# Performance work log

Hardware: AMD Instinct MI355X
Metric: run time of the kernel (lower is better)

The kernel has to match this reference:

```python
import jax, jax.numpy as jnp
import numpy as np


def _gru_dir(x, Wih, Whh, bih, bhh):
    # x: (B,T,I) -> (B,T,H); torch GRU equations, h0 = 0
    H = Whh.shape[1]
    pre = x @ Wih.T + bih  # (B,T,3H), input projection hoisted out of scan
    def step(h, p):
        gh = h @ Whh.T + bhh
        pr, pz, pn = jnp.split(p, 3, axis=-1)
        gr, gz, gn = jnp.split(gh, 3, axis=-1)
        r = jax.nn.sigmoid(pr + gr)
        z = jax.nn.sigmoid(pz + gz)
        n = jnp.tanh(pn + r * gn)
        h = (1.0 - z) * n + z * h
        return h, h
    h0 = jnp.zeros((x.shape[0], H), x.dtype)
    _, ys = jax.lax.scan(step, h0, jnp.swapaxes(pre, 0, 1))
    return jnp.swapaxes(ys, 0, 1)


def _gru_bidir(x, Wih, Whh, bih, bhh):
    f = _gru_dir(x, Wih[0], Whh[0], bih[0], bhh[0])
    b = _gru_dir(x[:, ::-1], Wih[1], Whh[1], bih[1], bhh[1])[:, ::-1]
    return jnp.concatenate([f, b], axis=-1)


def _forward(inputs, embed, l_Wih, l_Whh, l_bih, l_bhh, r_Wih, r_Whh, r_bih, r_bhh,
             a_Wih, a_Whh, a_bih, a_bhh, Wc1, Wc2, vc, Wb, Wd, vd, Wm, vm, Ws, vs,
             Wp, vp, Wpred):
    x = embed[inputs]  # (B,T,E)
    hl = _gru_bidir(x, l_Wih, l_Whh, l_bih, l_bhh)  # (B,T,2H)
    hr = _gru_bidir(x, r_Wih, r_Whh, r_bih, r_bhh)  # (B,T,2H)
    # co-attention: score[b,i,j] = vc . tanh(Wc1 hl_j + Wc2 hr_i)
    s = jnp.tanh((hl @ Wc1.T)[:, None, :, :] + (hr @ Wc2.T)[:, :, None, :])  # (B,T,T,H)
    ptc = jax.nn.softmax((s @ vc.T)[..., 0], axis=-1) @ hl
    # bilinear: hr (Wb hl)^T
    sjt = jnp.einsum('bid,bjd->bij', hr, hl @ Wb.T)
    ptb = jax.nn.softmax(sjt, axis=-1) @ hl
    # multiplicative: vd . tanh(Wd (hl_j * hr_i))
    p = hl[:, None, :, :] * hr[:, :, None, :]  # (B,T,T,2H)
    ptd = jax.nn.softmax((jnp.tanh(p @ Wd.T) @ vd.T)[..., 0], axis=-1) @ hl
    # subtractive: vm . tanh(Wm (hl_j - hr_i))
    d = hl[:, None, :, :] - hr[:, :, None, :]  # (B,T,T,2H)
    ptm = jax.nn.softmax((jnp.tanh(d @ Wm.T) @ vm.T)[..., 0], axis=-1) @ hl
    # self-attention on hr: vs . tanh(Ws (hr_j * hr_i))
    ss = hr[:, None, :, :] * hr[:, :, None, :]  # (B,T,T,2H)
    pts = jax.nn.softmax((jnp.tanh(ss @ Ws.T) @ vs.T)[..., 0], axis=-1) @ hr
    agg = jnp.concatenate([hr, pts, ptc, ptd, ptb, ptm], axis=-1)  # (B,T,12H)
    ar = _gru_bidir(agg, a_Wih, a_Whh, a_bih, a_bhh)  # (B,T,2H)
    # pooling of hl
    sj = jax.nn.softmax(jnp.swapaxes(jnp.tanh(hl @ Wp.T) @ vp.T, 1, 2), axis=-1)  # (B,1,T)
    rl = sj @ hl  # (B,1,2H)
    # final attention over aggregation
    sj2 = jax.nn.softmax(jnp.swapaxes((ar @ Wc1.T + rl @ Wc2.T) @ vc.T, 1, 2), axis=-1)  # (B,1,T)
    rr = (sj2 @ ar)[:, 0, :]  # (B,2H)
    return jax.nn.sigmoid(rr @ Wpred.T)  # (B,labels)


def setup_inputs() -> dict:
    B, T, V, E, H, L = 4, 256, 30000, 300, 128, 2
    key = jax.random.key(0)
    ks = jax.random.split(key, 40)
    inp = {}
    inp['inputs'] = jax.random.randint(ks[0], (B, T), 0, V)
    inp['embed'] = jax.random.uniform(ks[1], (V, E), jnp.float32, -0.1, 0.1)
    ki = 2
    for name, isz in [('l', E), ('r', E), ('a', 12 * H)]:
        inp[name + '_Wih'] = jax.random.normal(ks[ki], (2, 3 * H, isz), jnp.float32) * 0.05; ki += 1
        inp[name + '_Whh'] = jax.random.normal(ks[ki], (2, 3 * H, H), jnp.float32) * 0.05; ki += 1
        inp[name + '_bih'] = jnp.zeros((2, 3 * H), jnp.float32)
        inp[name + '_bhh'] = jnp.zeros((2, 3 * H), jnp.float32)
    for n, o, i in [('Wc1', H, 2 * H), ('Wc2', H, 2 * H), ('vc', 1, H), ('Wb', 2 * H, 2 * H),
                    ('Wd', H, 2 * H), ('vd', 1, H), ('Wm', H, 2 * H), ('vm', 1, H),
                    ('Ws', H, 2 * H), ('vs', 1, H), ('Wp', H, 2 * H), ('vp', 1, H),
                    ('Wpred', L, 2 * H)]:
        inp[n] = jax.random.normal(ks[ki], (o, i), jnp.float32) * 0.05; ki += 1
    return inp


def reference(inputs, embed, l_Wih, l_Whh, l_bih, l_bhh, r_Wih, r_Whh, r_bih, r_bhh,
              a_Wih, a_Whh, a_bih, a_bhh, Wc1, Wc2, vc, Wb, Wd, vd, Wm, vm, Ws, vs,
              Wp, vp, Wpred):
    return _forward(inputs, embed, l_Wih, l_Whh, l_bih, l_bhh, r_Wih, r_Whh, r_bih,
                    r_bhh, a_Wih, a_Whh, a_bih, a_bhh, Wc1, Wc2, vc, Wb, Wd, vd, Wm,
                    vm, Ws, vs, Wp, vp, Wpred)
```

## Files before the change

### kernel.cpp

```cpp
#include <hip/hip_runtime.h>


#define DEV static __device__ __forceinline__
#define BAR_LGKM() __asm__ volatile("s_waitcnt lgkmcnt(0)\ns_barrier" ::: "memory")

typedef __attribute__((ext_vector_type(4))) float f32x4;
typedef __attribute__((ext_vector_type(8))) short s16x8;
typedef __attribute__((ext_vector_type(4))) unsigned int u32x4;

constexpr int T = 256, E = 300, EP = 320, H = 128, H2 = 256, H3 = 384, H12 = 1536;
constexpr int M = 1024;
constexpr int STY = 262144;

DEV float b2f(unsigned short h) { return __uint_as_float(((unsigned)h) << 16); }
DEV unsigned short f2b(float f) {
  unsigned u = __float_as_uint(f);
  u += 0x7fff + ((u >> 16) & 1);
  return (unsigned short)(u >> 16);
}
DEV unsigned cvt_pk_bf16(float lo, float hi) {
  unsigned r;
  __asm__("v_cvt_pk_bf16_f32 %0, %1, %2" : "=v"(r) : "v"(lo), "v"(hi));
  return r;
}
DEV float rcp_f(float x) {
  float r;
  __asm__("v_rcp_f32 %0, %1" : "=v"(r) : "v"(x));
  return r;
}
DEV float sigm(float x) { return rcp_f(1.f + __expf(-x)); }
DEV float tanh_f(float x) {
  float e = __expf(2.f * x);
  return __builtin_fmaf(-2.f, rcp_f(e + 1.f), 1.f);
}

DEV s16x8 ldfrag(const unsigned short* p) {
  u32x4 v = *(const u32x4*)p;
  return __builtin_bit_cast(s16x8, v);
}
DEV f32x4 mfma16(s16x8 a, s16x8 b, f32x4 c) {
  return __builtin_amdgcn_mfma_f32_16x16x32_bf16(a, b, c, 0, 0, 0);
}


struct StageArgs {
  const float* cs[9]; unsigned short* cd[9]; int cn[9];
  const int* idx; const float* emb; unsigned short* xhi; unsigned short* xlo;
  const float* lW; const float* rW; unsigned short* wpad;
};

__global__ void k_stage(StageArgs sa) {
  int seg = blockIdx.y;
  int i = blockIdx.x * 256 + threadIdx.x;
  if (seg < 9) {
    if (i < sa.cn[seg]) sa.cd[seg][i] = f2b(sa.cs[seg][i]);
    return;
  }
  if (seg == 9) {
    if (i >= M * EP) return;
    int m = i / EP, e = i - m * EP;
    int r = sa.idx[m];
    float v = (e < E) ? sa.emb[(size_t)r * E + e] : 0.f;
    unsigned short hi = f2b(v);
    sa.xhi[i] = hi;
    sa.xlo[i] = f2b(v - b2f(hi));
    return;
  }
  if (i >= 4 * H3 * EP) return;
  int e = i % EP, n = (i / EP) % H3, uu = i / (EP * H3);
  const float* src = (uu < 2 ? sa.lW : sa.rW) + (size_t)((uu & 1) * H3 + n) * E;
  sa.wpad[i] = (e < E) ? f2b(src[e]) : (unsigned short)0;
}


struct GemmDesc {
  const unsigned short* Ahi; const unsigned short* Alo; const unsigned short* W;
  const float* bias; float* Cf; int N; int K; int tr;
};
struct GemmBatch { GemmDesc d[8]; };

__global__ __launch_bounds__(256) void k_gemm(GemmBatch gb) {
  GemmDesc g = gb.d[blockIdx.z];
  int nb = blockIdx.y * 64;
  if (nb >= g.N) return;
  int mb = blockIdx.x * 64;
  int lane = threadIdx.x & 63, w = threadIdx.x >> 6, quad = lane >> 4, l16 = lane & 15;
  int K = g.K;
  const unsigned short* Ahp = g.Ahi + (size_t)(mb + w * 16 + l16) * K + quad * 8;
  const unsigned short* Alp = g.Alo + (size_t)(mb + w * 16 + l16) * K + quad * 8;
  const unsigned short* Wp = g.W + (size_t)(nb + l16) * K + quad * 8;
  f32x4 acc[4];
  #pragma unroll
  for (int nt = 0; nt < 4; ++nt) acc[nt] = f32x4{0.f, 0.f, 0.f, 0.f};
  for (int k = 0; k < K; k += 32) {
    s16x8 ah = ldfrag(Ahp + k);
    s16x8 al = ldfrag(Alp + k);
    #pragma unroll
    for (int nt = 0; nt < 4; ++nt) {
      s16x8 b = ldfrag(Wp + (size_t)nt * 16 * K + k);
      acc[nt] = mfma16(ah, b, acc[nt]);
      acc[nt] = mfma16(al, b, acc[nt]);
    }
  }
  int mr0 = mb + w * 16 + quad * 4;
  #pragma unroll
  for (int nt = 0; nt < 4; ++nt) {
    int col = nb + nt * 16 + l16;
    float bv = g.bias ? g.bias[col] : 0.f;
    #pragma unroll
    for (int r = 0; r < 4; ++r) {
      if (g.tr)
        g.Cf[(size_t)col * M + (mr0 + r)] = acc[nt][r] + bv;
      else
        g.Cf[(size_t)(mr0 + r) * g.N + col] = acc[nt][r] + bv;
    }
  }
}


struct RecArgs {
  const unsigned short* whh[4];
  const float* pre[4];
  float* outf[4];
  unsigned short* outhi[4];
  unsigned short* outlo[4];
  unsigned short* agghi[4];
  unsigned short* agglo[4];
  const float* bhh[4];
  int colOff[4];
  int dir[4];
};

__global__ __launch_bounds__(512) void k_gru(RecArgs ra) {
  int u = blockIdx.x;
  __shared__ __align__(16) unsigned short hs[2][16 * 136];
  int tid = threadIdx.x, lane = tid & 63, w8 = tid >> 6;
  int quad = lane >> 4, l16 = lane & 15;
  for (int i = tid; i < 2 * 16 * 136; i += 512) ((unsigned short*)hs)[i] = 0;
  const unsigned short* whh = ra.whh[u];
  s16x8 bq[3][4];
  #pragma unroll
  for (int g = 0; g < 3; ++g) {
    int row = g * 128 + w8 * 16 + l16;
    #pragma unroll
    for (int kc = 0; kc < 4; ++kc)
      bq[g][kc] = ldfrag(whh + (size_t)row * H + kc * 32 + quad * 8);
  }
  const float* bhh = ra.bhh[u];
  const float* pre = ra.pre[u];
  float* outf = ra.outf[u];
  unsigned short* outhi = ra.outhi[u];
  unsigned short* outlo = ra.outlo[u];
  unsigned short* agghi = ra.agghi[u];
  unsigned short* agglo = ra.agglo[u];
  int colOff = ra.colOff[u], dir = ra.dir[u];
  int b = ((quad & 1) << 1) | (quad >> 1);
  int d = w8 * 16 + l16;
  float bh_r = bhh[d], bh_z = bhh[d + 128], bh_n = bhh[d + 256];
  float hf = 0.f;
  float ob[8];
  unsigned short obh[8], obl[8];
  int t0 = dir ? (T - 1) : 0;
  const float* pq = pre + (size_t)(b * T + t0) * H3 + d;
  float n_pr = pq[0], n_pz = pq[128], n_pn = pq[256];
  long pst = dir ? -(long)H3 : (long)H3;
  __syncthreads();
  for (int sb = 0; sb < T; sb += 8) {
    #pragma unroll
    for (int ss = 0; ss < 8; ++ss) {
      float pr = n_pr, pz = n_pz, pn = n_pn;
      pq += pst;
      n_pr = pq[0]; n_pz = pq[128]; n_pn = pq[256];
      const unsigned short* hcur = hs[ss & 1];
      unsigned short* hnxt = hs[(ss & 1) ^ 1];
      s16x8 ah[4];
      #pragma unroll
      for (int kc = 0; kc < 4; ++kc)
        ah[kc] = ldfrag(hcur + l16 * 136 + kc * 32 + quad * 8);
      f32x4 accA[3], accB[3];
      #pragma unroll
      for (int g = 0; g < 3; ++g) {
        accA[g] = f32x4{0.f, 0.f, 0.f, 0.f};
        accB[g] = f32x4{0.f, 0.f, 0.f, 0.f};
      }
      #pragma unroll
      for (int g = 0; g < 3; ++g) accA[g] = mfma16(ah[0], bq[g][0], accA[g]);
      #pragma unroll
      for (int g = 0; g < 3; ++g) accB[g] = mfma16(ah[2], bq[g][2], accB[g]);
      #pragma unroll
      for (int g = 0; g < 3; ++g) accA[g] = mfma16(ah[1], bq[g][1], accA[g]);
      #pragma unroll
      for (int g = 0; g < 3; ++g) accB[g] = mfma16(ah[3], bq[g][3], accB[g]);
      float ghv[3];
      #pragma unroll
      for (int g = 0; g < 3; ++g) {
        float x0 = (accA[g][0] + accB[g][0]) + (accA[g][1] + accB[g][1]);
        float x1 = (accA[g][2] + accB[g][2]) + (accA[g][3] + accB[g][3]);
        float y1 = __shfl_xor(x1, 32);
        ghv[g] = (quad >= 2) ? y1 : x0;
      }
      float rg = sigm(pr + ghv[0] + bh_r);
      float zg = sigm(pz + ghv[1] + bh_z);
      float ng = tanh_f(pn + rg * (ghv[2] + bh_n));
      hf = (1.f - zg) * ng + zg * hf;
      unsigned short hi = f2b(hf);
      unsigned short lo = f2b(hf - b2f(hi));
      hnxt[(2 * b) * 136 + d] = hi;
      hnxt[(2 * b + 1) * 136 + d] = lo;
      ob[ss] = hf; obh[ss] = hi; obl[ss] = lo;
      BAR_LGKM();
    }
    #pragma unroll
    for (int qq = 0; qq < 8; ++qq) {
      int sq = sb + qq;
      int tq = dir ? (T - 1 - sq) : sq;
      size_t o = (size_t)(b * T + tq) * H2 + colOff + d;
      outf[o] = ob[qq]; outhi[o] = obh[qq]; outlo[o] = obl[qq];
      if (agghi) {
        size_t a = (size_t)(b * T + tq) * H12 + colOff + d;
        agghi[a] = obh[qq]; agglo[a] = obl[qq];
      }
    }
  }
}


struct ScMMArgs {
  const unsigned short* Xhi[2];
  const float* Rf; const float* Wt[2]; const float* vt[2];
  float* So[2]; float* So2[2];
};

__global__ __launch_bounds__(256, 2) void k_scmm(ScMMArgs a) {
  __shared__ __align__(16) unsigned short w_lds[64 * 256];
  int which = blockIdx.y;
  int bi = blockIdx.x, b = bi >> 8;
  int tid = threadIdx.x;
  int type = which >> 1, khb = which & 1;
  const unsigned short* Xhi = a.Xhi[type];
  const float* W = a.Wt[type] + (size_t)khb * 64 * 256;
  const float* v = a.vt[type] + khb * 64;
  float* Sout = khb ? a.So2[type] : a.So[type];
  int lane = tid & 63, w = tid >> 6, quad = lane >> 4, l16 = lane & 15;
  int d4 = tid & 63, rhi = tid >> 6;
  float4 h4 = ((const float4*)(a.Rf + (size_t)bi * 256))[d4];
  #pragma unroll
  for (int it = 0; it < 16; ++it) {
    int kl = it * 4 + rhi;
    float4 w4 = ((const float4*)(W + (size_t)kl * 256))[d4];
    unsigned lo32 = cvt_pk_bf16(w4.x * h4.x, w4.y * h4.y);
    unsigned hi32 = cvt_pk_bf16(w4.z * h4.z, w4.w * h4.w);
    unsigned long long pk = (unsigned long long)lo32 | ((unsigned long long)hi32 << 32);
    int gphys = ((d4 >> 1) + kl) & 31;
    *(unsigned long long*)(w_lds + (size_t)kl * 256 + gphys * 8 + (d4 & 1) * 4) = pk;
  }
  BAR_LGKM();
  f32x4 acc[4][4];
  #pragma unroll
  for (int jj = 0; jj < 4; ++jj)
    #pragma unroll
    for (int c = 0; c < 4; ++c) acc[jj][c] = f32x4{0.f, 0.f, 0.f, 0.f};
  const unsigned short* Xp0 =
      Xhi + (size_t)(b * 256 + w * 4 * 16 + l16) * 256 + quad * 8;
  #pragma unroll 2
  for (int kc = 0; kc < 8; ++kc) {
    s16x8 af[4];
    #pragma unroll
    for (int c = 0; c < 4; ++c) {
      int krow = c * 16 + l16;
      int gp = (kc * 4 + quad + krow) & 31;
      af[c] = ldfrag(w_lds + (size_t)krow * 256 + gp * 8);
    }
    s16x8 bf[4];
    #pragma unroll
    for (int jj = 0; jj < 4; ++jj)
      bf[jj] = ldfrag(Xp0 + (size_t)jj * 16 * 256 + kc * 32);
    #pragma unroll
    for (int jj = 0; jj < 4; ++jj)
      #pragma unroll
      for (int c = 0; c < 4; ++c)
        acc[jj][c] = mfma16(af[c], bf[jj], acc[jj][c]);
  }
  float vv[4][4];
  #pragma unroll
  for (int c = 0; c < 4; ++c)
    #pragma unroll
    for (int r = 0; r < 4; ++r) vv[c][r] = v[c * 16 + quad * 4 + r];
  #pragma unroll
  for (int jj = 0; jj < 4; ++jj) {
    float s = 0.f;
    #pragma unroll
    for (int c = 0; c < 4; ++c)
      #pragma unroll
      for (int r = 0; r < 4; ++r) s += tanh_f(acc[jj][c][r]) * vv[c][r];
    s += __shfl_xor(s, 16);
    s += __shfl_xor(s, 32);
    int jt = w * 4 + jj;
    if (lane < 16) Sout[(size_t)bi * 256 + jt * 16 + l16] = s;
  }
}


struct ScCmbArgs {
  const float *Hc, *Rc, *Hm, *Rm, *HB, *hrf, *vcf, *vmf; float* S;
};

__global__ __launch_bounds__(256, 2) void k_sccmb(ScCmbArgs a) {
  int bi = blockIdx.x;
  int tid = threadIdx.x;
  __shared__ float rc_l[8 * 128];
  __shared__ float rm_l[8 * 128];
  __shared__ float hr_l[8 * 256];
  __shared__ float vc_l[128], vm_l[128];
  int b = bi >> 5, i0 = (bi & 31) << 3;
  int gi0 = b * 256 + i0;
  {
    const float4* rc4 = (const float4*)(a.Rc + (size_t)gi0 * 128);
    const float4* rm4 = (const float4*)(a.Rm + (size_t)gi0 * 128);
    ((float4*)rc_l)[tid] = rc4[tid];
    ((float4*)rm_l)[tid] = rm4[tid];
    const float4* hr4 = (const float4*)(a.hrf + (size_t)gi0 * 256);
    ((float4*)hr_l)[tid] = hr4[tid];
    ((float4*)hr_l)[256 + tid] = hr4[256 + tid];
    if (tid < 128) { vc_l[tid] = a.vcf[tid]; vm_l[tid] = a.vmf[tid]; }
  }
  __syncthreads();
  int j = tid;
  size_t cb = (size_t)(b * 256 + j);
  float scq[8], smq[8], sbq[8];
  #pragma unroll
  for (int q = 0; q < 8; ++q) { scq[q] = 0.f; smq[q] = 0.f; sbq[q] = 0.f; }
  for (int k = 0; k < 128; ++k) {
    float hc = a.Hc[(size_t)k * M + cb];
    float hm = a.Hm[(size_t)k * M + cb];
    float vck = vc_l[k], vmk = vm_l[k];
    #pragma unroll
    for (int q = 0; q < 8; ++q) {
      scq[q] += vck * tanh_f(hc + rc_l[q * 128 + k]);
      smq[q] += vmk * tanh_f(hm - rm_l[q * 128 + k]);
    }
  }
  for (int k = 0; k < 256; ++k) {
    float hb = a.HB[(size_t)k * M + cb];
    #pragma unroll
    for (int q = 0; q < 8; ++q) sbq[q] += hb * hr_l[q * 256 + k];
  }
  #pragma unroll
  for (int q = 0; q < 8; ++q) {
    size_t o = (size_t)(gi0 + q) * 256 + j;
    a.S[(size_t)STY * 1 + o] = scq[q];
    a.S[(size_t)STY * 3 + o] = sbq[q];
    a.S[(size_t)STY * 4 + o] = smq[q];
  }
}


__global__ __launch_bounds__(256) void k_wsum(const float* __restrict__ S,
    const float* __restrict__ S2,
    const float* __restrict__ hl_f, const float* __restrict__ hr_f,
    unsigned short* __restrict__ ahi, unsigned short* __restrict__ alo) {
  int it = blockIdx.x, type = blockIdx.y, b = blockIdx.z;
  __shared__ float p_l[8][256];
  __shared__ float red[4];
  int tid = threadIdx.x;
  for (int ii = 0; ii < 8; ++ii) {
    size_t idx = ((size_t)(b * 256 + it * 8 + ii)) * 256 + tid;
    float x = S[(size_t)type * STY + idx];
    if (type == 0) x += S2[idx];
    else if (type == 2) x += S2[(size_t)STY + idx];
    float m = x;
    for (int dl = 32; dl; dl >>= 1) m = fmaxf(m, __shfl_xor(m, dl));
    if ((tid & 63) == 0) red[tid >> 6] = m;
    __syncthreads();
    m = fmaxf(fmaxf(red[0], red[1]), fmaxf(red[2], red[3]));
    __syncthreads();
    float e = __expf(x - m);
    float sum = e;
    for (int dl = 32; dl; dl >>= 1) sum += __shfl_xor(sum, dl);
    if ((tid & 63) == 0) red[tid >> 6] = sum;
    __syncthreads();
    sum = red[0] + red[1] + red[2] + red[3];
    p_l[ii][tid] = e * rcp_f(sum);
    __syncthreads();
  }
  const float* src = (type == 0 ? hr_f : hl_f) + (size_t)b * 256 * 256;
  float acc[8] = {0.f, 0.f, 0.f, 0.f, 0.f, 0.f, 0.f, 0.f};
  for (int j = 0; j < 256; ++j) {
    float hv = src[(size_t)j * 256 + tid];
    #pragma unroll
    for (int ii = 0; ii < 8; ++ii) acc[ii] += p_l[ii][j] * hv;
  }
  int off = 256 * (1 + type);
  #pragma unroll
  for (int ii = 0; ii < 8; ++ii) {
    float vv = acc[ii];
    unsigned short hi = f2b(vv);
    size_t o = (size_t)(b * 256 + it * 8 + ii) * H12 + off + tid;
    ahi[o] = hi;
    alo[o] = f2b(vv - b2f(hi));
  }
}


__global__ __launch_bounds__(256) void k_tail(const float* __restrict__ Hp,
    const float* __restrict__ hl_f, const float* __restrict__ vpf,
    const float* __restrict__ Wc2f, const float* __restrict__ Arc,
    const float* __restrict__ ar_f, const float* __restrict__ vcf,
    const float* __restrict__ Wpredf, float* __restrict__ out) {
  int b = blockIdx.x, tid = threadIdx.x;
  __shared__ float vl[128], wl[256], rvec[256], rlcl[128], red[4];
  if (tid < 128) vl[tid] = vpf[tid];
  __syncthreads();
  const float* hp = Hp + (size_t)(b * 256 + tid) * 128;
  float s = 0.f;
  for (int k = 0; k < 128; ++k) s += vl[k] * tanh_f(hp[k]);
  float m = s;
  for (int dl = 32; dl; dl >>= 1) m = fmaxf(m, __shfl_xor(m, dl));
  if ((tid & 63) == 0) red[tid >> 6] = m;
  __syncthreads();
  m = fmaxf(fmaxf(red[0], red[1]), fmaxf(red[2], red[3]));
  __syncthreads();
  float e = __expf(s - m);
  float sum = e;
  for (int dl = 32; dl; dl >>= 1) sum += __shfl_xor(sum, dl);
  if ((tid & 63) == 0) red[tid >> 6] = sum;
  __syncthreads();
  sum = red[0] + red[1] + red[2] + red[3];
  wl[tid] = e * rcp_f(sum);
  __syncthreads();
  float acc = 0.f;
  for (int t = 0; t < 256; ++t) acc += wl[t] * hl_f[(size_t)(b * 256 + t) * 256 + tid];
  rvec[tid] = acc;
  __syncthreads();
  if (tid < 128) {
    float a2 = 0.f;
    const float* wr = Wc2f + (size_t)tid * 256;
    for (int dk = 0; dk < 256; ++dk) a2 += rvec[dk] * wr[dk];
    rlcl[tid] = a2;
    vl[tid] = vcf[tid];
  }
  __syncthreads();
  const float* ap = Arc + (size_t)(b * 256 + tid) * 128;
  float s2 = 0.f;
  for (int k = 0; k < 128; ++k) s2 += vl[k] * (ap[k] + rlcl[k]);
  m = s2;
  for (int dl = 32; dl; dl >>= 1) m = fmaxf(m, __shfl_xor(m, dl));
  if ((tid & 63) == 0) red[tid >> 6] = m;
  __syncthreads();
  m = fmaxf(fmaxf(red[0], red[1]), fmaxf(red[2], red[3]));
  __syncthreads();
  float e2 = __expf(s2 - m);
  float sum2 = e2;
  for (int dl = 32; dl; dl >>= 1) sum2 += __shfl_xor(sum2, dl);
  if ((tid & 63) == 0) red[tid >> 6] = sum2;
  __syncthreads();
  sum2 = red[0] + red[1] + red[2] + red[3];
  wl[tid] = e2 * rcp_f(sum2);
  __syncthreads();
  float acc2 = 0.f;
  for (int t = 0; t < 256; ++t) acc2 += wl[t] * ar_f[(size_t)(b * 256 + t) * 256 + tid];
  rvec[tid] = acc2;
  __syncthreads();
  if (tid < 2) {
    float o = 0.f;
    const float* wp = Wpredf + (size_t)tid * 256;
    for (int dk = 0; dk < 256; ++dk) o += rvec[dk] * wp[dk];
    out[b * 2 + tid] = sigm(o);
  }
}


extern "C" void kernel_launch(void* const* d_in, const int* in_sizes, int n_in,
                              void* d_out, int out_size, void* d_ws, size_t ws_size,
                              hipStream_t stream) {
  (void)in_sizes; (void)n_in; (void)out_size; (void)ws_size;
  const int* inputs = (const int*)d_in[0];
  const float* embed = (const float*)d_in[1];
  const float* lWih = (const float*)d_in[2];
  const float* lWhh = (const float*)d_in[3];
  const float* lbih = (const float*)d_in[4];
  const float* lbhh = (const float*)d_in[5];
  const float* rWih = (const float*)d_in[6];
  const float* rWhh = (const float*)d_in[7];
  const float* rbih = (const float*)d_in[8];
  const float* rbhh = (const float*)d_in[9];
  const float* aWih = (const float*)d_in[10];
  const float* aWhh = (const float*)d_in[11];
  const float* abih = (const float*)d_in[12];
  const float* abhh = (const float*)d_in[13];
  const float* Wc1 = (const float*)d_in[14];
  const float* Wc2 = (const float*)d_in[15];
  const float* vc  = (const float*)d_in[16];
  const float* Wb  = (const float*)d_in[17];
  const float* Wd  = (const float*)d_in[18];
  const float* vd  = (const float*)d_in[19];
  const float* Wm  = (const float*)d_in[20];
  const float* vmv = (const float*)d_in[21];
  const float* Wsw = (const float*)d_in[22];
  const float* vsv = (const float*)d_in[23];
  const float* Wp  = (const float*)d_in[24];
  const float* vp  = (const float*)d_in[25];
  const float* Wpred = (const float*)d_in[26];

  char* ws = (char*)d_ws;
  size_t off = 0;
  auto alloc = [&](size_t bytes) -> void* {
    void* p = ws + off;
    off += (bytes + 255) & ~(size_t)255;
    return p;
  };
  unsigned short* xhi = (unsigned short*)alloc((size_t)M * EP * 2);
  unsigned short* xlo = (unsigned short*)alloc((size_t)M * EP * 2);
  unsigned short* wpad = (unsigned short*)alloc((size_t)4 * H3 * EP * 2);
  unsigned short* Whh_b = (unsigned short*)alloc((size_t)6 * H3 * H * 2);
  unsigned short* aWih_b = (unsigned short*)alloc((size_t)2 * H3 * H12 * 2);
  unsigned short* Wc1_b = (unsigned short*)alloc((size_t)H * H2 * 2);
  unsigned short* Wc2_b = (unsigned short*)alloc((size_t)H * H2 * 2);
  unsigned short* Wm_b  = (unsigned short*)alloc((size_t)H * H2 * 2);
  unsigned short* Wp_b  = (unsigned short*)alloc((size_t)H * H2 * 2);
  unsigned short* Wb_b  = (unsigned short*)alloc((size_t)H2 * H2 * 2);
  char* region1 = (char*)alloc((size_t)4 * M * H3 * 4);
  float* pre_lr = (float*)region1;
  float* S      = (float*)region1;
  float* pre_a  = (float*)region1;
  float* S2 = (float*)alloc((size_t)2 * STY * 4);
  float* hl_f = (float*)alloc((size_t)M * H2 * 4);
  float* hr_f = (float*)alloc((size_t)M * H2 * 4);
  unsigned short* hl_hi = (unsigned short*)alloc((size_t)M * H2 * 2);
  unsigned short* hl_lo = (unsigned short*)alloc((size_t)M * H2 * 2);
  unsigned short* hr_hi = (unsigned short*)alloc((size_t)M * H2 * 2);
  unsigned short* hr_lo = (unsigned short*)alloc((size_t)M * H2 * 2);
  float* Hc = (float*)alloc((size_t)M * H * 4);
  float* Rc = (float*)alloc((size_t)M * H * 4);
  float* Hm = (float*)alloc((size_t)M * H * 4);
  float* Rm = (float*)alloc((size_t)M * H * 4);
  float* Hp = (float*)alloc((size_t)M * H * 4);
  float* HB = (float*)alloc((size_t)M * H2 * 4);
  unsigned short* agg_hi = (unsigned short*)alloc((size_t)M * H12 * 2);
  unsigned short* agg_lo = (unsigned short*)alloc((size_t)M * H12 * 2);
  float* ar_f = (float*)alloc((size_t)M * H2 * 4);
  unsigned short* ar_hi = (unsigned short*)alloc((size_t)M * H2 * 2);
  unsigned short* ar_lo = (unsigned short*)alloc((size_t)M * H2 * 2);
  float* Arc = (float*)alloc((size_t)M * H * 4);

  StageArgs sa{};
  sa.cs[0] = lWhh;  sa.cd[0] = Whh_b;                 sa.cn[0] = 2 * H3 * H;
  sa.cs[1] = rWhh;  sa.cd[1] = Whh_b + 2 * H3 * H;    sa.cn[1] = 2 * H3 * H;
  sa.cs[2] = aWhh;  sa.cd[2] = Whh_b + 4 * H3 * H;    sa.cn[2] = 2 * H3 * H;
  sa.cs[3] = aWih;  sa.cd[3] = aWih_b;                sa.cn[3] = 2 * H3 * H12;
  sa.cs[4] = Wc1;   sa.cd[4] = Wc1_b;                 sa.cn[4] = H * H2;
  sa.cs[5] = Wc2;   sa.cd[5] = Wc2_b;                 sa.cn[5] = H * H2;
  sa.cs[6] = Wm;    sa.cd[6] = Wm_b;                  sa.cn[6] = H * H2;
  sa.cs[7] = Wp;    sa.cd[7] = Wp_b;                  sa.cn[7] = H * H2;
  sa.cs[8] = Wb;    sa.cd[8] = Wb_b;                  sa.cn[8] = H2 * H2;
  sa.idx = inputs; sa.emb = embed; sa.xhi = xhi; sa.xlo = xlo;
  sa.lW = lWih; sa.rW = rWih; sa.wpad = wpad;
  k_stage<<<dim3((2 * H3 * H12 + 255) / 256, 11), dim3(256), 0, stream>>>(sa);

  GemmBatch ga{};
  const float* biases[4] = { lbih, lbih + H3, rbih, rbih + H3 };
  for (int u = 0; u < 4; ++u)
    ga.d[u] = GemmDesc{ xhi, xlo, wpad + (size_t)u * H3 * EP, biases[u],
                        pre_lr + (size_t)u * M * H3, H3, EP, 0 };
  k_gemm<<<dim3(16, 6, 4), dim3(256), 0, stream>>>(ga);

  RecArgs r1{};
  r1.whh[0] = Whh_b;               r1.whh[1] = Whh_b + H3 * H;
  r1.whh[2] = Whh_b + 2 * H3 * H;  r1.whh[3] = Whh_b + 3 * H3 * H;
  for (int u = 0; u < 4; ++u) r1.pre[u] = pre_lr + (size_t)u * M * H3;
  r1.outf[0] = r1.outf[1] = hl_f; r1.outf[2] = r1.outf[3] = hr_f;
  r1.outhi[0] = r1.outhi[1] = hl_hi; r1.outhi[2] = r1.outhi[3] = hr_hi;
  r1.outlo[0] = r1.outlo[1] = hl_lo; r1.outlo[2] = r1.outlo[3] = hr_lo;
  r1.agghi[0] = r1.agghi[1] = nullptr; r1.agghi[2] = r1.agghi[3] = agg_hi;
  r1.agglo[0] = r1.agglo[1] = nullptr; r1.agglo[2] = r1.agglo[3] = agg_lo;
  r1.bhh[0] = lbhh; r1.bhh[1] = lbhh + H3; r1.bhh[2] = rbhh; r1.bhh[3] = rbhh + H3;
  r1.colOff[0] = 0; r1.colOff[1] = H; r1.colOff[2] = 0; r1.colOff[3] = H;
  r1.dir[0] = 0; r1.dir[1] = 1; r1.dir[2] = 0; r1.dir[3] = 1;
  k_gru<<<dim3(4), dim3(512), 0, stream>>>(r1);

  GemmBatch gbB{};
  gbB.d[0] = GemmDesc{ hl_hi, hl_lo, Wc1_b, nullptr, Hc, H, H2, 1 };
  gbB.d[1] = GemmDesc{ hr_hi, hr_lo, Wc2_b, nullptr, Rc, H, H2, 0 };
  gbB.d[2] = GemmDesc{ hl_hi, hl_lo, Wm_b, nullptr, Hm, H, H2, 1 };
  gbB.d[3] = GemmDesc{ hr_hi, hr_lo, Wm_b, nullptr, Rm, H, H2, 0 };
  gbB.d[4] = GemmDesc{ hl_hi, hl_lo, Wb_b, nullptr, HB, H2, H2, 1 };
  gbB.d[5] = GemmDesc{ hl_hi, hl_lo, Wp_b, nullptr, Hp, H, H2, 0 };
  k_gemm<<<dim3(16, 4, 6), dim3(256), 0, stream>>>(gbB);

  ScMMArgs sm{};
  sm.Xhi[0] = hl_hi; sm.Wt[0] = Wd;  sm.vt[0] = vd;  sm.So[0] = S + (size_t)2 * STY;
  sm.Xhi[1] = hr_hi; sm.Wt[1] = Wsw; sm.vt[1] = vsv; sm.So[1] = S + (size_t)0 * STY;
  sm.So2[0] = S2 + (size_t)STY;
  sm.So2[1] = S2;
  sm.Rf = hr_f;
  k_scmm<<<dim3(M, 4), dim3(256), 0, stream>>>(sm);

  ScCmbArgs scb{};
  scb.Hc = Hc; scb.Rc = Rc; scb.Hm = Hm; scb.Rm = Rm; scb.HB = HB;
  scb.hrf = hr_f; scb.vcf = vc; scb.vmf = vmv; scb.S = S;
  k_sccmb<<<dim3(128), dim3(256), 0, stream>>>(scb);

  k_wsum<<<dim3(32, 5, 4), dim3(256), 0, stream>>>(S, S2, hl_f, hr_f, agg_hi, agg_lo);

  GemmBatch gc{};
  gc.d[0] = GemmDesc{ agg_hi, agg_lo, aWih_b, abih, pre_a, H3, H12, 0 };
  gc.d[1] = GemmDesc{ agg_hi, agg_lo, aWih_b + (size_t)H3 * H12, abih + H3,
                      pre_a + (size_t)M * H3, H3, H12, 0 };
  k_gemm<<<dim3(16, 6, 2), dim3(256), 0, stream>>>(gc);

  RecArgs r2{};
  r2.whh[0] = Whh_b + 4 * H3 * H; r2.whh[1] = Whh_b + 5 * H3 * H;
  r2.whh[2] = r2.whh[3] = Whh_b + 4 * H3 * H;
  r2.pre[0] = pre_a; r2.pre[1] = pre_a + (size_t)M * H3;
  r2.pre[2] = r2.pre[3] = pre_a;
  r2.outf[0] = r2.outf[1] = r2.outf[2] = r2.outf[3] = ar_f;
  r2.outhi[0] = r2.outhi[1] = r2.outhi[2] = r2.outhi[3] = ar_hi;
  r2.outlo[0] = r2.outlo[1] = r2.outlo[2] = r2.outlo[3] = ar_lo;
  for (int u = 0; u < 4; ++u) { r2.agghi[u] = nullptr; r2.agglo[u] = nullptr; }
  r2.bhh[0] = abhh; r2.bhh[1] = abhh + H3; r2.bhh[2] = r2.bhh[3] = abhh;
  r2.colOff[0] = 0; r2.colOff[1] = H; r2.colOff[2] = r2.colOff[3] = 0;
  r2.dir[0] = 0; r2.dir[1] = 1; r2.dir[2] = r2.dir[3] = 0;
  k_gru<<<dim3(2), dim3(512), 0, stream>>>(r2);

  GemmBatch gd{};
  gd.d[0] = GemmDesc{ ar_hi, ar_lo, Wc1_b, nullptr, Arc, H, H2, 0 };
  k_gemm<<<dim3(16, 2, 1), dim3(256), 0, stream>>>(gd);

  k_tail<<<dim3(4), dim3(256), 0, stream>>>(Hp, hl_f, vp, Wc2, Arc, ar_f, vc, Wpred,
                                            (float*)d_out);
}
```

Before: 748.4 us.

## Restructure GRU recurrence step to overlap gate math with MFMAs and prefetch two steps

The recurrent GRU kernel now orders the MFMAs gate by gate, so the r-gate sigmoid can start while the z and n MFMAs are still in flight. The cross-half reduction uses permlane32_swap instead of a shuffle plus select, and the input biases are folded into the prefetched pre-activation loads. Loads are double-prefetched with separate even and odd pointers, and outputs are stored every step instead of being buffered over 8 steps. The intent is to shorten the serial per-step critical path. The cost is global stores issued inside the latency-bound loop before each barrier.

```diff
diff --git a/kernel.cpp b/kernel.cpp
--- a/kernel.cpp
+++ b/kernel.cpp
@@ -7,6 +7,7 @@
 typedef __attribute__((ext_vector_type(4))) float f32x4;
 typedef __attribute__((ext_vector_type(8))) short s16x8;
 typedef __attribute__((ext_vector_type(4))) unsigned int u32x4;
+typedef __attribute__((ext_vector_type(2))) unsigned int u32x2;
 
 constexpr int T = 256, E = 300, EP = 320, H = 128, H2 = 256, H3 = 384, H12 = 1536;
 constexpr int M = 1024;
@@ -32,6 +33,11 @@
 DEV float tanh_f(float x) {
   float e = __expf(2.f * x);
   return __builtin_fmaf(-2.f, rcp_f(e + 1.f), 1.f);
+}
+DEV float plsel(float x0, float x1) {
+  u32x2 r = __builtin_amdgcn_permlane32_swap(
+      __float_as_uint(x0), __float_as_uint(x1), false, false);
+  return __uint_as_float(r[0]);
 }
 
 DEV s16x8 ldfrag(const unsigned short* p) {
@@ -131,6 +137,53 @@
   int dir[4];
 };
 
+#define GRU_STEP(pr_, pz_, pn_, pq_, hcur_, hnxt_, s_)                         \
+  {                                                                            \
+    float pr = pr_, pz = pz_, pn = pn_;                                        \
+    pq_ += pst2;                                                               \
+    pr_ = pq_[0] + bh_r; pz_ = pq_[128] + bh_z; pn_ = pq_[256];                \
+    const unsigned short* hb_ = hcur_ + l16 * 136 + quad * 8;                  \
+    s16x8 ah0 = ldfrag(hb_);                                                   \
+    s16x8 ah1 = ldfrag(hb_ + 32);                                              \
+    s16x8 ah2 = ldfrag(hb_ + 64);                                              \
+    s16x8 ah3 = ldfrag(hb_ + 96);                                              \
+    f32x4 z4 = f32x4{0.f, 0.f, 0.f, 0.f};                                      \
+    f32x4 aR0 = mfma16(ah0, bq[0][0], z4);                                     \
+    f32x4 aR1 = mfma16(ah2, bq[0][2], z4);                                     \
+    aR0 = mfma16(ah1, bq[0][1], aR0);                                          \
+    aR1 = mfma16(ah3, bq[0][3], aR1);                                          \
+    f32x4 aZ0 = mfma16(ah0, bq[1][0], z4);                                     \
+    f32x4 aZ1 = mfma16(ah2, bq[1][2], z4);                                     \
+    aZ0 = mfma16(ah1, bq[1][1], aZ0);                                          \
+    aZ1 = mfma16(ah3, bq[1][3], aZ1);                                          \
+    float r0 = (aR0[0] + aR1[0]) + (aR0[1] + aR1[1]);                          \
+    float r1v = (aR0[2] + aR1[2]) + (aR0[3] + aR1[3]);                         \
+    float rg = sigm(pr + plsel(r0, r1v));                                      \
+    f32x4 aN0 = mfma16(ah0, bq[2][0], z4);                                     \
+    f32x4 aN1 = mfma16(ah2, bq[2][2], z4);                                     \
+    aN0 = mfma16(ah1, bq[2][1], aN0);                                          \
+    aN1 = mfma16(ah3, bq[2][3], aN1);                                          \
+    float z0 = (aZ0[0] + aZ1[0]) + (aZ0[1] + aZ1[1]);                          \
+    float z1 = (aZ0[2] + aZ1[2]) + (aZ0[3] + aZ1[3]);                          \
+    float zg = sigm(pz + plsel(z0, z1));                                       \
+    float n0 = (aN0[0] + aN1[0]) + (aN0[1] + aN1[1]);                          \
+    float n1 = (aN0[2] + aN1[2]) + (aN0[3] + aN1[3]);                          \
+    float ng = tanh_f(pn + rg * (plsel(n0, n1) + bh_n));                       \
+    hf = __builtin_fmaf(zg, hf - ng, ng);                                      \
+    unsigned short hi = f2b(hf);                                               \
+    unsigned short lo = f2b(hf - b2f(hi));                                     \
+    hnxt_[(2 * b) * 136 + d] = hi;                                             \
+    hnxt_[(2 * b + 1) * 136 + d] = lo;                                         \
+    int tq = dir ? (T - 1 - (s_)) : (s_);                                      \
+    size_t o_ = (size_t)(b * T + tq) * H2 + colOff + d;                        \
+    outf[o_] = hf; outhi[o_] = hi; outlo[o_] = lo;                             \
+    if (agghi) {                                                               \
+      size_t a_ = (size_t)(b * T + tq) * H12 + colOff + d;                     \
+      agghi[a_] = hi; agglo[a_] = lo;                                          \
+    }                                                                          \
+    BAR_LGKM();                                                                \
+  }
+
 __global__ __launch_bounds__(512) void k_gru(RecArgs ra) {
   int u = blockIdx.x;
   __shared__ __align__(16) unsigned short hs[2][16 * 136];
@@ -158,69 +211,17 @@
   int d = w8 * 16 + l16;
   float bh_r = bhh[d], bh_z = bhh[d + 128], bh_n = bhh[d + 256];
   float hf = 0.f;
-  float ob[8];
-  unsigned short obh[8], obl[8];
   int t0 = dir ? (T - 1) : 0;
-  const float* pq = pre + (size_t)(b * T + t0) * H3 + d;
-  float n_pr = pq[0], n_pz = pq[128], n_pn = pq[256];
   long pst = dir ? -(long)H3 : (long)H3;
-  __syncthreads();
-  for (int sb = 0; sb < T; sb += 8) {
-    #pragma unroll
-    for (int ss = 0; ss < 8; ++ss) {
-      float pr = n_pr, pz = n_pz, pn = n_pn;
-      pq += pst;
-      n_pr = pq[0]; n_pz = pq[128]; n_pn = pq[256];
-      const unsigned short* hcur = hs[ss & 1];
-      unsigned short* hnxt = hs[(ss & 1) ^ 1];
-      s16x8 ah[4];
-      #pragma unroll
-      for (int kc = 0; kc < 4; ++kc)
-        ah[kc] = ldfrag(hcur + l16 * 136 + kc * 32 + quad * 8);
-      f32x4 accA[3], accB[3];
-      #pragma unroll
-      for (int g = 0; g < 3; ++g) {
-        accA[g] = f32x4{0.f, 0.f, 0.f, 0.f};
-        accB[g] = f32x4{0.f, 0.f, 0.f, 0.f};
-      }
-      #pragma unroll
-      for (int g = 0; g < 3; ++g) accA[g] = mfma16(ah[0], bq[g][0], accA[g]);
-      #pragma unroll
-      for (int g = 0; g < 3; ++g) accB[g] = mfma16(ah[2], bq[g][2], accB[g]);
-      #pragma unroll
-      for (int g = 0; g < 3; ++g) accA[g] = mfma16(ah[1], bq[g][1], accA[g]);
-      #pragma unroll
-      for (int g = 0; g < 3; ++g) accB[g] = mfma16(ah[3], bq[g][3], accB[g]);
-      float ghv[3];
-      #pragma unroll
-      for (int g = 0; g < 3; ++g) {
-        float x0 = (accA[g][0] + accB[g][0]) + (accA[g][1] + accB[g][1]);
-        float x1 = (accA[g][2] + accB[g][2]) + (accA[g][3] + accB[g][3]);
-        float y1 = __shfl_xor(x1, 32);
-        ghv[g] = (quad >= 2) ? y1 : x0;
-      }
-      float rg = sigm(pr + ghv[0] + bh_r);
-      float zg = sigm(pz + ghv[1] + bh_z);
-      float ng = tanh_f(pn + rg * (ghv[2] + bh_n));
-      hf = (1.f - zg) * ng + zg * hf;
-      unsigned short hi = f2b(hf);
-      unsigned short lo = f2b(hf - b2f(hi));
-      hnxt[(2 * b) * 136 + d] = hi;
-      hnxt[(2 * b + 1) * 136 + d] = lo;
-      ob[ss] = hf; obh[ss] = hi; obl[ss] = lo;
-      BAR_LGKM();
-    }
-    #pragma unroll
-    for (int qq = 0; qq < 8; ++qq) {
-      int sq = sb + qq;
-      int tq = dir ? (T - 1 - sq) : sq;
-      size_t o = (size_t)(b * T + tq) * H2 + colOff + d;
-      outf[o] = ob[qq]; outhi[o] = obh[qq]; outlo[o] = obl[qq];
-      if (agghi) {
-        size_t a = (size_t)(b * T + tq) * H12 + colOff + d;
-        agghi[a] = obh[qq]; agglo[a] = obl[qq];
-      }
-    }
+  long pst2 = 2 * pst;
+  const float* pqE = pre + (size_t)(b * T + t0) * H3 + d;
+  const float* pqO = pqE + pst;
+  float e_pr = pqE[0] + bh_r, e_pz = pqE[128] + bh_z, e_pn = pqE[256];
+  float o_pr = pqO[0] + bh_r, o_pz = pqO[128] + bh_z, o_pn = pqO[256];
+  __syncthreads();
+  for (int s = 0; s < T; s += 2) {
+    GRU_STEP(e_pr, e_pz, e_pn, pqE, hs[0], hs[1], s);
+    GRU_STEP(o_pr, o_pz, o_pn, pqO, hs[1], hs[0], s + 1);
   }
 }
 
```

New measurement: 720.0 us. 3.8% less time.
